# Optimization experiments

Measured on AMD Instinct MI355X. Metric: run time of the kernel, lower is better.

## Reference

```python
import jax, jax.numpy as jnp
import numpy as np

KSIZE = 3; STRIDE = 1; RATE = 2; FUSE_K = 3; SCALE = 10.0; EPS = 1e-4
B, C, RH, RW = 2, 128, 80, 80  # raw (full-res) feature shape


def setup_inputs() -> dict:
    key = jax.random.key(0)
    ks = jax.random.split(key, 5)
    shp = (B, C, RH, RW)
    names = ["left", "right", "mid", "raw_left", "raw_right"]
    return {n: jax.random.normal(k, shp, dtype=jnp.float32) for n, k in zip(names, ks)}


def _same_pads(H, W, k, s):
    oh, ow = -(-H // s), -(-W // s)
    ph = max(0, (oh - 1) * s + k - H)
    pw = max(0, (ow - 1) * s + k - W)
    return ((ph // 2, ph - ph // 2), (pw // 2, pw - pw // 2))


def extract_patches(x, k, s):
    # torch extract_image_patches with 'same' padding -> (b, L, c, k, k)
    b, c, H, W = x.shape
    pads = _same_pads(H, W, k, s)
    p = jax.lax.conv_general_dilated_patches(x, (k, k), (s, s), pads)  # (b, c*k*k, oh, ow)
    oh, ow = p.shape[2], p.shape[3]
    p = p.reshape(b, c, k, k, oh * ow)  # feature dim is channel-major (c, k, k), like torch unfold
    return p.transpose(0, 4, 1, 2, 3)


def _fuse(s, Hl, Wl, Hm, Wm):
    # diagonal fuse-conv: conv of (b,1,L,P) score image with eye(k), twice with transposes
    b = s.shape[0]
    k = FUSE_K
    eye = jnp.eye(k, dtype=s.dtype).reshape(1, 1, k, k)
    pad = ((k // 2, k // 2), (k // 2, k // 2))
    conv = lambda x: jax.lax.conv_general_dilated(x, eye, (1, 1), pad)
    x = conv(s.reshape(b, 1, Hl * Wl, Hm * Wm))
    x = x.reshape(b, Hl, Wl, Hm, Wm).transpose(0, 2, 1, 4, 3).reshape(b, 1, Wl * Hl, Wm * Hm)
    x = conv(x)
    x = x.reshape(b, Wl, Hl, Wm, Hm).transpose(0, 2, 1, 4, 3)  # (b, Hl, Wl, Hm, Wm)
    return x.reshape(b, Hl * Wl, Hm, Wm)


def _deconv_one(attn, patches):
    # torch conv_transpose2d(attn, patches, stride=RATE, padding=1):
    # conv with lhs dilation RATE, spatially-flipped kernel, padding k-1-1
    kk = patches.shape[-1]
    rhs = jnp.flip(patches, (-2, -1)).transpose(1, 0, 2, 3)  # (C, L, kk, kk)
    p = kk - 1 - 1
    out = jax.lax.conv_general_dilated(attn[None], rhs, (1, 1), ((p, p), (p, p)),
                                       lhs_dilation=(RATE, RATE),
                                       dimension_numbers=('NCHW', 'OIHW', 'NCHW'))
    return out[0]


def _forward(left, right, mid, raw_left, raw_right):
    kernel = 2 * RATE
    rawp_l = extract_patches(raw_left, kernel, RATE * STRIDE)   # (B, L, C, 4, 4)
    rawp_r = extract_patches(raw_right, kernel, RATE * STRIDE)
    # nearest downsample by rate
    l = left[:, :, ::RATE, ::RATE]
    r = right[:, :, ::RATE, ::RATE]
    m = mid[:, :, ::RATE, ::RATE]
    Hl, Wl = l.shape[2], l.shape[3]
    Hm, Wm = m.shape[2], m.shape[3]
    lp = extract_patches(l, KSIZE, STRIDE)   # (B, L, C, 3, 3)
    rp = extract_patches(r, KSIZE, STRIDE)
    mp = extract_patches(m, KSIZE, STRIDE)   # (B, P, C, 3, 3); conv2d(same-padded xi, w) == patch dot

    def norm(p):
        # torch: sqrt(reduce_sum(p^2 + eps)) -- eps added elementwise before the sum
        return p / jnp.sqrt(jnp.sum(p * p + EPS, axis=(2, 3, 4), keepdims=True))

    sl = jnp.einsum('bqcij,bpcij->bqp', norm(lp), mp).reshape(-1, Hl * Wl, Hm, Wm)
    sr = jnp.einsum('bqcij,bpcij->bqp', norm(rp), mp).reshape(-1, Hl * Wl, Hm, Wm)
    sl = _fuse(sl, Hl, Wl, Hm, Wm)
    sr = _fuse(sr, Hl, Wl, Hm, Wm)
    al = jax.nn.softmax(sl * SCALE, axis=1)
    ar = jax.nn.softmax(sr * SCALE, axis=1)
    y_l = jax.vmap(_deconv_one)(al, rawp_l) / 4.0   # (B, C, RH, RW)
    y_r = jax.vmap(_deconv_one)(ar, rawp_r) / 4.0
    # cos_function_weight: cosine blending ramp along width (1 at left edge -> 0 at right edge)
    w = 0.5 * (1.0 + jnp.cos(jnp.pi * jnp.arange(RW, dtype=y_l.dtype) / (RW - 1)))
    w = w.reshape(1, 1, 1, RW)
    return w * y_l + jnp.flip(w, 3) * y_r


def reference(left, right, mid, raw_left, raw_right):
    return _forward(left, right, mid, raw_left, raw_right)
```

## Files before the change

### kernel.cpp

```cpp
#include <hip/hip_runtime.h>
#include <hip/hip_bf16.h>

typedef __hip_bfloat16 bf16;
typedef __attribute__((ext_vector_type(8))) short short8;
typedef __attribute__((ext_vector_type(4))) float f32x4;
typedef unsigned short ushort_t;

#define PI_F 3.14159265358979323846f
#define GPAD_Z 3111696L

#define GLOAD_LDS16(gp, lp)                                                    \
  __builtin_amdgcn_global_load_lds(                                            \
      (const __attribute__((address_space(1))) unsigned int*)(gp),             \
      (__attribute__((address_space(3))) unsigned int*)(lp), 16, 0, 0)

__global__ __launch_bounds__(128) void prep_pt(const float* __restrict__ left,
                                               const float* __restrict__ right,
                                               const float* __restrict__ mid,
                                               bf16* __restrict__ PTe,
                                               bf16* __restrict__ MTe,
                                               float* __restrict__ SQ) {
  int q = blockIdx.x;
  int y = blockIdx.y;
  int c = threadIdx.x;
  int qi = q / 40, qj = q - qi * 40;
  const float* src;
  bf16* dst;
  int b;
  bool aside = (y < 4);
  if (aside) {
    b = y & 1;
    src = (y < 2) ? left : right;
    dst = PTe + (long)y * 1664 * 384;
  } else {
    b = y - 4;
    src = mid;
    dst = MTe + (long)(y - 4) * 1664 * 384;
  }
  float v = src[(((long)b * 128 + c) * 80 + 2 * qi) * 80 + 2 * qj];
  bf16 hi = __float2bfloat16(v);
  bf16 lo = __float2bfloat16(v - __bfloat162float(hi));
  if (aside) {
    dst[(long)q * 384 + c] = hi;
    dst[(long)q * 384 + 128 + c] = lo;
    dst[(long)q * 384 + 256 + c] = hi;
  } else {
    dst[(long)q * 384 + c] = hi;
    dst[(long)q * 384 + 128 + c] = hi;
    dst[(long)q * 384 + 256 + c] = lo;
  }
  if (aside) {
    __shared__ float red[128];
    red[c] = v * v;
    __syncthreads();
    for (int s = 64; s > 0; s >>= 1) {
      if (c < s) red[c] += red[c + s];
      __syncthreads();
    }
    if (c == 0) SQ[y * 1600 + q] = red[0];
  }
}

__global__ void invn_kernel(const float* __restrict__ SQ, float* __restrict__ INV) {
  int idx = blockIdx.x * 256 + threadIdx.x;
  if (idx >= 6400) return;
  int z = idx / 1600, q = idx - z * 1600;
  int qi = q / 40, qj = q - qi * 40;
  float s = 0.1152f;
  #pragma unroll
  for (int di = -1; di <= 1; ++di)
    #pragma unroll
    for (int dj = -1; dj <= 1; ++dj) {
      int a = qi + di, b = qj + dj;
      if (a >= 0 && a < 40 && b >= 0 && b < 40) s += SQ[z * 1600 + a * 40 + b];
    }
  INV[idx] = rsqrtf(s);
}

__global__ __launch_bounds__(256) void padzero_kernel(float* __restrict__ Gp) {
  int row = blockIdx.x;
  int z = blockIdx.y;
  float* R = Gp + (long)z * GPAD_Z + (long)row * 1764;
  int r42 = row % 42;
  if (r42 == 0 || r42 == 41) {
    for (int c = threadIdx.x; c < 1764; c += 256) R[c] = 0.f;
  } else {
    for (int i = threadIdx.x; i < 84; i += 256) {
      int c = (i >> 1) * 42 + ((i & 1) ? 41 : 0);
      R[c] = 0.f;
    }
  }
}

__global__ __launch_bounds__(256) void gemm_nt(const bf16* __restrict__ A,
                                               const bf16* __restrict__ B,
                                               float* __restrict__ C,
                                               int M, int N, int K,
                                               long Az, long Bz, long Cz,
                                               int bmod, int cpad) {
  int z = blockIdx.z;
  A += (long)z * Az;
  B += (long)(bmod ? (z & 1) : z) * Bz;
  C += (long)z * Cz;
  __shared__ bf16 As[128 * 32];
  __shared__ bf16 Bs[128 * 32];
  int lane = threadIdx.x & 63;
  int w = threadIdx.x >> 6;
  int mb = blockIdx.x * 128;
  int nb = blockIdx.y * 128;
  int lr = lane >> 2;
  int gb = (lane & 3) ^ ((lane >> 3) & 3);
  int lm = lane & 15;
  int swz = (lm >> 1) & 3;
  int kb = lane >> 4;
  int pos = (kb ^ swz) * 8;
  int warow = (w >> 1) * 64;
  int wbrow = (w & 1) * 64;
  f32x4 acc[4][4];
  #pragma unroll
  for (int i = 0; i < 4; ++i)
    #pragma unroll
    for (int j = 0; j < 4; ++j) {
      f32x4 zv = {0.f, 0.f, 0.f, 0.f};
      acc[i][j] = zv;
    }
  for (int k0 = 0; k0 < K; k0 += 32) {
    __syncthreads();
    #pragma unroll
    for (int t = 0; t < 2; ++t) {
      int r = (w * 2 + t) * 16 + lr;
      GLOAD_LDS16(A + (long)(mb + r) * K + k0 + gb * 8, As + (w * 2 + t) * 512);
      GLOAD_LDS16(B + (long)(nb + r) * K + k0 + gb * 8, Bs + (w * 2 + t) * 512);
    }
    __syncthreads();
    short8 af[4], bfr[4];
    #pragma unroll
    for (int i = 0; i < 4; ++i) {
      af[i]  = *reinterpret_cast<const short8*>(As + (warow + i * 16 + lm) * 32 + pos);
      bfr[i] = *reinterpret_cast<const short8*>(Bs + (wbrow + i * 16 + lm) * 32 + pos);
    }
    #pragma unroll
    for (int i = 0; i < 4; ++i)
      #pragma unroll
      for (int j = 0; j < 4; ++j)
        acc[i][j] = __builtin_amdgcn_mfma_f32_16x16x32_bf16(af[i], bfr[j], acc[i][j], 0, 0, 0);
  }
  int m0 = mb + warow;
  int n0 = nb + wbrow;
  int col = lane & 15;
  int r0 = (lane >> 4) * 4;
  #pragma unroll
  for (int i = 0; i < 4; ++i)
    #pragma unroll
    for (int j = 0; j < 4; ++j) {
      int n = n0 + j * 16 + col;
      if (n < N) {
        int nc = cpad ? ((n / 40) * 42 + (n - (n / 40) * 40) + 43) : n;
        #pragma unroll
        for (int r = 0; r < 4; ++r) {
          int m = m0 + i * 16 + r0 + r;
          if (m < M) {
            long mr = cpad ? ((long)((m / 40) * 42 + (m - (m / 40) * 40) + 43) * 1764)
                           : ((long)m * N);
            C[mr + nc] = acc[i][j][r];
          }
        }
      }
    }
}

__global__ __launch_bounds__(256) void s1fuse1_kernel(const float* __restrict__ Gp,
                                                      const float* __restrict__ INV,
                                                      float* __restrict__ S2) {
  int p = blockIdx.x * 256 + threadIdx.x;
  if (p >= 1600) return;
  int q = blockIdx.y, z = blockIdx.z;
  const float* Gz = Gp + (long)z * GPAD_Z;
  float s = 0.f;
  #pragma unroll
  for (int d = -1; d <= 1; ++d) {
    int q2 = q + d, p2 = p + d;
    bool ok = ((unsigned)q2 < 1600u) && ((unsigned)p2 < 1600u);
    int q2c = ok ? q2 : 0;
    int p2c = ok ? p2 : 0;
    float wgt = ok ? INV[z * 1600 + q2c] : 0.f;
    int qi = q2c / 40, qj = q2c - qi * 40;
    int pi = p2c / 40, pj = p2c - pi * 40;
    const float* base = Gz + (long)(qi * 42 + qj + 43) * 1764 + (pi * 42 + pj + 43);
    float t = 0.f;
    #pragma unroll
    for (int di = -1; di <= 1; ++di)
      #pragma unroll
      for (int dj = -1; dj <= 1; ++dj)
        t += base[(long)(di * 42 + dj) * 1765];
    s += t * wgt;
  }
  S2[((long)z * 1600 + q) * 1600 + p] = s;
}

__global__ __launch_bounds__(256) void fuse2_kernel(const float* __restrict__ S2,
                                                    float* __restrict__ S3) {
  int p = blockIdx.x * 256 + threadIdx.x;
  if (p >= 1600) return;
  int q = blockIdx.y, z = blockIdx.z;
  const float* S = S2 + (long)z * 2560000;
  int il = q / 40, jl = q - il * 40;
  int im = p / 40, jm = p - im * 40;
  int u = jl * 40 + il, v = jm * 40 + im;
  float s = 0.f;
  #pragma unroll
  for (int d = -1; d <= 1; ++d) {
    int u2 = u + d, v2 = v + d;
    if (u2 >= 0 && u2 < 1600 && v2 >= 0 && v2 < 1600) {
      int q2 = (u2 % 40) * 40 + u2 / 40;
      int p2 = (v2 % 40) * 40 + v2 / 40;
      s += S[(long)q2 * 1600 + p2];
    }
  }
  S3[((long)z * 1600 + q) * 1600 + p] = s;
}

__global__ __launch_bounds__(256) void smax_part(const float* __restrict__ S3,
                                                 float* __restrict__ Pm,
                                                 float* __restrict__ Ps) {
  int z = blockIdx.z, qc = blockIdx.y;
  int pl = threadIdx.x & 63;
  int ql = threadIdx.x >> 6;
  int p = blockIdx.x * 64 + pl;
  const float* S = S3 + (long)z * 2560000;
  float m = -1e30f, s = 0.f;
  for (int i = 0; i < 50; ++i) {
    int q = qc * 200 + i * 4 + ql;
    float x = 10.f * S[(long)q * 1600 + p];
    if (x > m) { s *= __expf(m - x); m = x; }
    s += __expf(x - m);
  }
  __shared__ float lm[4][64], ls[4][64];
  lm[ql][pl] = m;
  ls[ql][pl] = s;
  __syncthreads();
  if (ql == 0) {
    float M = m, SS = s;
    #pragma unroll
    for (int j = 1; j < 4; ++j) {
      float mj = lm[j][pl], sj = ls[j][pl];
      if (mj > M) { SS = SS * __expf(M - mj) + sj; M = mj; }
      else SS += sj * __expf(mj - M);
    }
    Pm[((long)z * 8 + qc) * 1600 + p] = M;
    Ps[((long)z * 8 + qc) * 1600 + p] = SS;
  }
}

__global__ __launch_bounds__(256) void smax_write(const float* __restrict__ S3,
                                                  const float* __restrict__ Pm,
                                                  const float* __restrict__ Ps,
                                                  bf16* __restrict__ AT) {
  int z = blockIdx.z;
  int p0 = blockIdx.x * 64, q0 = blockIdx.y * 64;
  int pl = threadIdx.x & 63, ql = threadIdx.x >> 6;
  __shared__ float lfm[64], lfs[64];
  if (ql == 0) {
    int p = p0 + pl;
    float M = -1e30f;
    #pragma unroll
    for (int c = 0; c < 8; ++c) M = fmaxf(M, Pm[((long)z * 8 + c) * 1600 + p]);
    float S = 0.f;
    #pragma unroll
    for (int c = 0; c < 8; ++c)
      S += Ps[((long)z * 8 + c) * 1600 + p] * __expf(Pm[((long)z * 8 + c) * 1600 + p] - M);
    lfm[pl] = M;
    lfs[pl] = 1.f / S;
  }
  __syncthreads();
  __shared__ ushort_t T[64][66];
  float fm = lfm[pl];
  float fs = lfs[pl];
  const float* S = S3 + (long)z * 2560000;
  #pragma unroll
  for (int i = 0; i < 16; ++i) {
    int qq = ql + i * 4;
    float x = 10.f * S[(long)(q0 + qq) * 1600 + p0 + pl];
    bf16 h = __float2bfloat16(__expf(x - fm) * fs);
    T[pl][qq] = *reinterpret_cast<ushort_t*>(&h);
  }
  __syncthreads();
  int rp = threadIdx.x >> 5;
  int j = threadIdx.x & 31;
  #pragma unroll
  for (int pass = 0; pass < 8; ++pass) {
    int row = pass * 8 + rp;
    unsigned int vv = (unsigned int)T[row][2 * j] | ((unsigned int)T[row][2 * j + 1] << 16);
    *reinterpret_cast<unsigned int*>(AT + ((long)z * 1664 + p0 + row) * 1600 + q0 + 2 * j) = vv;
  }
}

__global__ __launch_bounds__(256) void rawpt_kernel(const float* __restrict__ rawL,
                                                    const float* __restrict__ rawR,
                                                    bf16* __restrict__ RAWPT) {
  int z = blockIdx.z;
  int r = blockIdx.y * 4 + (threadIdx.x >> 6);
  int q = blockIdx.x * 64 + (threadIdx.x & 63);
  const float* raw = ((z < 2) ? rawL : rawR) + (long)(z & 1) * 819200;
  int c = r >> 4, i = (r >> 2) & 3, j = r & 3;
  int qi = q / 40, qj = q - qi * 40;
  int y = 2 * qi + i - 1, x = 2 * qj + j - 1;
  float v = 0.f;
  if (y >= 0 && y < 80 && x >= 0 && x < 80) v = raw[((long)c * 80 + y) * 80 + x];
  RAWPT[((long)z * 2048 + r) * 1600 + q] = __float2bfloat16(v);
}

__global__ __launch_bounds__(256) void paste_kernel(const float* __restrict__ Z,
                                                    float* __restrict__ out) {
  int idx = blockIdx.x * 256 + threadIdx.x;
  int x = idx % 80;
  int t = idx / 80;
  int y = t % 80;
  t /= 80;
  int c = t % 128;
  int b = t / 128;
  int imA = (y - 1) >> 1, ipA = y - 2 * imA + 1;
  int jmA = (x - 1) >> 1, jpA = x - 2 * jmA + 1;
  const long zs = 2048L * 1600;
  const float* ZL = Z + (long)b * zs;
  const float* ZR = Z + (long)(2 + b) * zs;
  float aL = 0.f, aR = 0.f;
  #pragma unroll
  for (int a = 0; a < 2; ++a) {
    int im = imA + a, ip = ipA - 2 * a;
    if (im < 0 || im > 39) continue;
    #pragma unroll
    for (int e = 0; e < 2; ++e) {
      int jm = jmA + e, jp = jpA - 2 * e;
      if (jm < 0 || jm > 39) continue;
      long off = (long)((c << 4) + ip * 4 + jp) * 1600 + im * 40 + jm;
      aL += ZL[off];
      aR += ZR[off];
    }
  }
  float wx = 0.5f * (1.f + cosf(PI_F * x / 79.f));
  float wf = 0.5f * (1.f + cosf(PI_F * (79 - x) / 79.f));
  out[idx] = 0.25f * (wx * aL + wf * aR);
}

extern "C" void kernel_launch(void* const* d_in, const int* in_sizes, int n_in,
                              void* d_out, int out_size, void* d_ws, size_t ws_size,
                              hipStream_t stream) {
  const float* left  = (const float*)d_in[0];
  const float* right = (const float*)d_in[1];
  const float* mid   = (const float*)d_in[2];
  const float* rawL  = (const float*)d_in[3];
  const float* rawR  = (const float*)d_in[4];
  float* out = (float*)d_out;
  char* ws = (char*)d_ws;

  bf16*  PTe   = (bf16*)(ws + 0);
  bf16*  MTe   = (bf16*)(ws + 5111808);
  float* SQ    = (float*)(ws + 7667712);
  float* INV   = (float*)(ws + 7693312);
  float* Pm    = (float*)(ws + 7718912);
  float* Ps    = (float*)(ws + 7923712);
  float* X     = (float*)(ws + 8179712);
  float* Y     = (float*)(ws + 60608512);
  bf16*  AT    = (bf16*)(ws + 101568512);
  bf16*  RAWPT = (bf16*)Y;

  prep_pt<<<dim3(1600, 6, 1), 128, 0, stream>>>(left, right, mid, PTe, MTe, SQ);
  invn_kernel<<<25, 256, 0, stream>>>(SQ, INV);
  padzero_kernel<<<dim3(1764, 4), 256, 0, stream>>>(X);
  gemm_nt<<<dim3(13, 13, 4), 256, 0, stream>>>(PTe, MTe, X, 1600, 1600, 384,
                                               1664L * 384, 1664L * 384, GPAD_Z, 1, 1);
  s1fuse1_kernel<<<dim3(7, 1600, 4), 256, 0, stream>>>(X, INV, Y);
  fuse2_kernel<<<dim3(7, 1600, 4), 256, 0, stream>>>(Y, X);
  smax_part<<<dim3(25, 8, 4), 256, 0, stream>>>(X, Pm, Ps);
  smax_write<<<dim3(25, 25, 4), 256, 0, stream>>>(X, Pm, Ps, AT);
  rawpt_kernel<<<dim3(25, 512, 4), 256, 0, stream>>>(rawL, rawR, RAWPT);
  gemm_nt<<<dim3(16, 13, 4), 256, 0, stream>>>(RAWPT, AT, X, 2048, 1600, 1600,
                                               2048L * 1600, 1664L * 1600, 2048L * 1600, 0, 0);
  paste_kernel<<<6400, 256, 0, stream>>>(X, out);
}
```

Baseline: 354.9 us.

## Add 256x256-tile double-buffered MFMA GEMM for the deconvolution matmul

Adds a new bf16 GEMM kernel with 256x256 output tiles and 512 threads. It stages A/B through 128KB of LDS using direct global-to-LDS loads with XOR swizzling and double buffering, and interleaves quarter-tile MFMA phases with barriers and setprio. The kernel replaces the 64-tile-style gemm_nt for the final 2048x1600x1600 deconvolution GEMM, aiming for more data reuse per tile and overlap of loads with compute. The trade-offs are large LDS use limiting occupancy, and only 224 blocks, which leaves the device underfilled. Out-of-range N rows are clamped to the padded allocation.

```diff
diff --git a/kernel.cpp b/kernel.cpp
--- a/kernel.cpp
+++ b/kernel.cpp
@@ -169,6 +169,132 @@
     }
 }
 
+#define BAR() __builtin_amdgcn_s_barrier()
+#define LGKM0() asm volatile("s_waitcnt lgkmcnt(0)" ::: "memory")
+#define STAGE_A(tt, h)                                                         \
+  { long _k = (long)(tt) * 64;                                                 \
+    char* _d = lds + (((tt) & 1) << 16) + (((h) * 8 + w) << 11);               \
+    GLOAD_LDS16(a_row[h] + _k, _d);                                            \
+    GLOAD_LDS16(a_row[h] + _k + 32, _d + 1024); }
+#define STAGE_B(tt, h)                                                         \
+  { long _k = (long)(tt) * 64;                                                 \
+    char* _d = lds + (((tt) & 1) << 16) + 32768 + (((h) * 8 + w) << 11);       \
+    GLOAD_LDS16(b_row[h] + _k, _d);                                            \
+    GLOAD_LDS16(b_row[h] + _k + 32, _d + 1024); }
+#define LD8(off) (*reinterpret_cast<const short8*>(lds + (off)))
+#define LOAD_A(bufo, mh)                                                       \
+  { _Pragma("unroll") for (int i = 0; i < 4; ++i)                              \
+      { _Pragma("unroll") for (int kc = 0; kc < 2; ++kc)                       \
+          a[i][kc] = LD8((bufo) + (((wm * 8 + (mh) * 4 + i) * 2 + kc) << 10) + rd_off); } }
+#define LOAD_B(dst, bufo, nh)                                                  \
+  { _Pragma("unroll") for (int j = 0; j < 2; ++j)                              \
+      { _Pragma("unroll") for (int kc = 0; kc < 2; ++kc)                       \
+          dst[j][kc] = LD8((bufo) + 32768 + (((wn * 4 + (nh) * 2 + j) * 2 + kc) << 10) + rd_off); } }
+#define MFMA16(mh, nh, bset)                                                   \
+  { _Pragma("unroll") for (int kc = 0; kc < 2; ++kc)                           \
+      { _Pragma("unroll") for (int i = 0; i < 4; ++i)                          \
+          { _Pragma("unroll") for (int j = 0; j < 2; ++j)                      \
+              acc[(mh) * 4 + i][(nh) * 2 + j] = __builtin_amdgcn_mfma_f32_16x16x32_bf16( \
+                  a[i][kc], bset[j][kc], acc[(mh) * 4 + i][(nh) * 2 + j], 0, 0, 0); } } }
+
+__global__ __launch_bounds__(512, 2) void gemm256_nt(const bf16* __restrict__ A,
+                                                     const bf16* __restrict__ B,
+                                                     float* __restrict__ C,
+                                                     int M, int N, int K,
+                                                     long Az, long Bz, long Cz,
+                                                     int nballoc) {
+  __shared__ __align__(16) char lds[131072];
+  int z = blockIdx.z;
+  A += (long)z * Az;
+  B += (long)z * Bz;
+  C += (long)z * Cz;
+  int tid = threadIdx.x;
+  int lane = tid & 63;
+  int w = tid >> 6;
+  int wm = w >> 2;
+  int wn = w & 3;
+  int mb = blockIdx.x * 256;
+  int nb = blockIdx.y * 256;
+  int NT = K >> 6;
+
+  int srcb = (lane << 4) ^ (lane & 32);
+  int r_src = srcb >> 6;
+  int c_src = (srcb & 63) >> 1;
+  const bf16* a_row[2];
+  const bf16* b_row[2];
+  #pragma unroll
+  for (int h = 0; h < 2; ++h) {
+    a_row[h] = A + (long)(mb + (h * 8 + w) * 16 + r_src) * K + c_src;
+    int br = nb + (h * 8 + w) * 16 + r_src;
+    if (br > nballoc - 1) br = nballoc - 1;
+    b_row[h] = B + (long)br * K + c_src;
+  }
+  int rd_off = (((lane & 15) << 6) | ((lane >> 4) << 4)) ^ ((lane & 8) << 2);
+
+  short8 a[4][2], p0[2][2], p1[2][2];
+  f32x4 acc[8][4];
+  #pragma unroll
+  for (int i = 0; i < 8; ++i)
+    #pragma unroll
+    for (int j = 0; j < 4; ++j) {
+      f32x4 zv = {0.f, 0.f, 0.f, 0.f};
+      acc[i][j] = zv;
+    }
+
+  STAGE_A(0, 0); STAGE_A(0, 1); STAGE_B(0, 0); STAGE_B(0, 1);
+  STAGE_A(1, 0); STAGE_A(1, 1); STAGE_B(1, 0);
+  asm volatile("s_waitcnt vmcnt(6)" ::: "memory");
+  BAR();
+
+  for (int t = 0; t < NT; ++t) {
+    int bufo = (t & 1) << 16;
+    LOAD_A(bufo, 0);
+    LOAD_B(p0, bufo, 0);
+    if (t + 1 < NT) STAGE_B(t + 1, 1);
+    BAR(); LGKM0();
+    __builtin_amdgcn_s_setprio(1); MFMA16(0, 0, p0); __builtin_amdgcn_s_setprio(0);
+    BAR();
+    LOAD_B(p1, bufo, 1);
+    BAR(); LGKM0();
+    __builtin_amdgcn_s_setprio(1); MFMA16(0, 1, p1); __builtin_amdgcn_s_setprio(0);
+    BAR();
+    LOAD_A(bufo, 1);
+    BAR(); LGKM0();
+    __builtin_amdgcn_s_setprio(1); MFMA16(1, 1, p1); __builtin_amdgcn_s_setprio(0);
+    BAR();
+    LOAD_B(p0, bufo, 0);
+    BAR(); LGKM0();
+    __builtin_amdgcn_s_setprio(1); MFMA16(1, 0, p0); __builtin_amdgcn_s_setprio(0);
+    BAR();
+    if (t + 2 < NT) {
+      STAGE_A(t + 2, 0); STAGE_A(t + 2, 1); STAGE_B(t + 2, 0);
+      asm volatile("s_waitcnt vmcnt(6)" ::: "memory");
+      BAR();
+    } else if (t + 1 < NT) {
+      asm volatile("s_waitcnt vmcnt(0)" ::: "memory");
+      BAR();
+    }
+  }
+
+  int col = lane & 15;
+  int r0 = (lane >> 4) * 4;
+  int m_base = mb + wm * 128;
+  int n_base = nb + wn * 64;
+  #pragma unroll
+  for (int i = 0; i < 8; ++i)
+    #pragma unroll
+    for (int j = 0; j < 4; ++j) {
+      int n = n_base + j * 16 + col;
+      if (n < N) {
+        #pragma unroll
+        for (int r = 0; r < 4; ++r) {
+          int m = m_base + i * 16 + r0 + r;
+          C[(long)m * N + n] = acc[i][j][r];
+        }
+      }
+    }
+}
+
 __global__ __launch_bounds__(256) void s1fuse1_kernel(const float* __restrict__ Gp,
                                                       const float* __restrict__ INV,
                                                       float* __restrict__ S2) {
@@ -375,7 +501,7 @@
   smax_part<<<dim3(25, 8, 4), 256, 0, stream>>>(X, Pm, Ps);
   smax_write<<<dim3(25, 25, 4), 256, 0, stream>>>(X, Pm, Ps, AT);
   rawpt_kernel<<<dim3(25, 512, 4), 256, 0, stream>>>(rawL, rawR, RAWPT);
-  gemm_nt<<<dim3(16, 13, 4), 256, 0, stream>>>(RAWPT, AT, X, 2048, 1600, 1600,
-                                               2048L * 1600, 1664L * 1600, 2048L * 1600, 0, 0);
+  gemm256_nt<<<dim3(8, 7, 4), 512, 0, stream>>>(RAWPT, AT, X, 2048, 1600, 1600,
+                                                2048L * 1600, 1664L * 1600, 2048L * 1600, 1664);
   paste_kernel<<<6400, 256, 0, stream>>>(X, out);
 }
```

Result: faster. 340.3 us (-4.1%).
